# Performance work log

Measured on AMD Instinct MI355X. Metric: run time of the kernel, lower is better.

## Reference

```python
import jax, jax.numpy as jnp
import numpy as np

N, K, M, D = 50000, 32, 50000, 128  # dst nodes, neighbors, src nodes, hidden_dim


def setup_inputs() -> dict:
    key = jax.random.key(0)
    k1, k2, k3, k4 = jax.random.split(key, 4)
    nei = jax.random.randint(k1, (N, K), 0, M, dtype=jnp.int64)
    h = jax.random.normal(k2, (M, D), dtype=jnp.float32)
    h_refer = jax.random.normal(k3, (N, D), dtype=jnp.float32)
    # xavier_normal_ on (1, 2D) with gain=1.414: std = gain*sqrt(2/(1+2D))
    std = 1.414 * np.sqrt(2.0 / (1 + 2 * D))
    att = jax.random.normal(k4, (1, 2 * D), dtype=jnp.float32) * std
    return {"nei": nei, "h": h, "h_refer": h_refer, "att": att}


def reference(nei, h, h_refer, att):
    # gather neighbor embeddings: [N, K, D]
    nei_emb = h[nei]
    # split att so we never materialize the concatenated [N, K, 2D] tensor:
    # cat([h_refer, nei_emb], -1) @ att.T == h_refer @ att_ref + nei_emb @ att_nei
    att_ref = att[0, :D]   # [D]
    att_nei = att[0, D:]   # [D]
    scores = (h_refer @ att_ref)[:, None] + jnp.einsum("nkd,d->nk", nei_emb, att_nei)  # [N, K]
    scores = jax.nn.leaky_relu(scores, negative_slope=0.01)
    w = jax.nn.softmax(scores, axis=1)  # softmax over neighbors
    # weighted sum over neighbors -> [N, D]
    return jnp.einsum("nk,nkd->nd", w, nei_emb)
```

## Files before the change

kernel.cpp:

```cpp
#include <hip/hip_runtime.h>

typedef unsigned int uint32;
typedef unsigned long long uint64;
typedef unsigned short ushort_t;
typedef _Float16 h2_t __attribute__((ext_vector_type(2)));
typedef float  f32x2 __attribute__((ext_vector_type(2)));
typedef float  f32x4 __attribute__((ext_vector_type(4)));
typedef uint32 u32x2 __attribute__((ext_vector_type(2)));

#define KNEI 32
#define DIM 128
#define WPB 4
#define RPW 2
#define WAVE_LDS 8192

enum { SRC_BF16 = 0, SRC_F16 = 1, SRC_F32 = 2 };

__device__ __forceinline__ float bflo(uint32 u) {
    union { uint32 u; float f; } c; c.u = u << 16; return c.f;
}
__device__ __forceinline__ float bfhi(uint32 u) {
    union { uint32 u; float f; } c; c.u = u & 0xffff0000u; return c.f;
}
__device__ __forceinline__ uint32 pack_bf16_rne(float a, float b) {
    union { float f; uint32 u; } x, y; x.f = a; y.f = b;
    uint32 ua = (x.u + 0x7fffu + ((x.u >> 16) & 1u)) >> 16;
    uint32 ub = (y.u + 0x7fffu + ((y.u >> 16) & 1u)) >> 16;
    return (ua & 0xffffu) | (ub << 16);
}
__device__ __forceinline__ uint32 pack_f16(float a, float b) {
    union { h2_t h; uint32 u; } c;
    c.h.x = (_Float16)a; c.h.y = (_Float16)b;
    return c.u;
}
__device__ __forceinline__ h2_t as_h2(uint32 u) {
    union { uint32 u; h2_t h; } c; c.u = u; return c.h;
}

__device__ __forceinline__ void prefetch16(const void* g, void* l) {
    __builtin_amdgcn_global_load_lds(
        (const __attribute__((address_space(1))) void*)g,
        (__attribute__((address_space(3))) void*)l,
        16, 0, 0);
}

__device__ __forceinline__ bool probe_bf16(const void* h, int lane) {
    const uint32 hs = ((const uint32*)h)[lane];
    const uint32 e  = (hs >> 7) & 0xFFu;
    const bool  tb  = (e >= 90u) && (e <= 140u);
    return (__ballot(tb) == ~0ull);
}

template<int SRC>
__device__ __forceinline__ float dot8(const uint4 e, const float* an) {
    if constexpr (SRC == SRC_BF16) {
        return bflo(e.x) * an[0] + bfhi(e.x) * an[1]
             + bflo(e.y) * an[2] + bfhi(e.y) * an[3]
             + bflo(e.z) * an[4] + bfhi(e.z) * an[5]
             + bflo(e.w) * an[6] + bfhi(e.w) * an[7];
    } else {
        const h2_t e0 = as_h2(e.x), e1 = as_h2(e.y), e2 = as_h2(e.z), e3 = as_h2(e.w);
        const float t0 = fmaf((float)e0.x, an[0],
                         fmaf((float)e0.y, an[1],
                         fmaf((float)e1.x, an[2], (float)e1.y * an[3])));
        const float t1 = fmaf((float)e2.x, an[4],
                         fmaf((float)e2.y, an[5],
                         fmaf((float)e3.x, an[6], (float)e3.y * an[7])));
        return t0 + t1;
    }
}

template<int SRC>
__device__ __forceinline__ void acc8(float* acc, float wk, const uint4 e) {
    if constexpr (SRC == SRC_BF16) {
        acc[0] = fmaf(wk, bflo(e.x), acc[0]);
        acc[1] = fmaf(wk, bfhi(e.x), acc[1]);
        acc[2] = fmaf(wk, bflo(e.y), acc[2]);
        acc[3] = fmaf(wk, bfhi(e.y), acc[3]);
        acc[4] = fmaf(wk, bflo(e.z), acc[4]);
        acc[5] = fmaf(wk, bfhi(e.z), acc[5]);
        acc[6] = fmaf(wk, bflo(e.w), acc[6]);
        acc[7] = fmaf(wk, bfhi(e.w), acc[7]);
    } else {
        const h2_t e0 = as_h2(e.x), e1 = as_h2(e.y), e2 = as_h2(e.z), e3 = as_h2(e.w);
        acc[0] = fmaf(wk, (float)e0.x, acc[0]);
        acc[1] = fmaf(wk, (float)e0.y, acc[1]);
        acc[2] = fmaf(wk, (float)e1.x, acc[2]);
        acc[3] = fmaf(wk, (float)e1.y, acc[3]);
        acc[4] = fmaf(wk, (float)e2.x, acc[4]);
        acc[5] = fmaf(wk, (float)e2.y, acc[5]);
        acc[6] = fmaf(wk, (float)e3.x, acc[6]);
        acc[7] = fmaf(wk, (float)e3.y, acc[7]);
    }
}

template<int SRC>
__device__ __forceinline__ f32x2 process_row(
    const uint4* ev, const float* an, float base, int r4)
{
    float s[8];
    #pragma unroll
    for (int it = 0; it < 8; ++it) s[it] = dot8<SRC>(ev[it], an);
    #pragma unroll
    for (int off = 1; off <= 8; off <<= 1) {
        #pragma unroll
        for (int it = 0; it < 8; ++it)
            s[it] += __shfl_xor(s[it], off, 64);
    }
    #pragma unroll
    for (int it = 0; it < 8; ++it) {
        const float v = base + s[it];
        s[it] = (v > 0.f) ? v : 0.01f * v;
    }

    float m = fmaxf(fmaxf(fmaxf(s[0], s[1]), fmaxf(s[2], s[3])),
                    fmaxf(fmaxf(s[4], s[5]), fmaxf(s[6], s[7])));
    m = fmaxf(m, __shfl_xor(m, 16, 64));
    m = fmaxf(m, __shfl_xor(m, 32, 64));

    float w[8];
    #pragma unroll
    for (int it = 0; it < 8; ++it) w[it] = __expf(s[it] - m);
    float sum = ((w[0] + w[1]) + (w[2] + w[3])) + ((w[4] + w[5]) + (w[6] + w[7]));
    sum += __shfl_xor(sum, 16, 64);
    sum += __shfl_xor(sum, 32, 64);
    const float inv = 1.0f / sum;

    float acc[8] = {0.f, 0.f, 0.f, 0.f, 0.f, 0.f, 0.f, 0.f};
    #pragma unroll
    for (int it = 0; it < 8; ++it)
        acc8<SRC>(acc, w[it] * inv, ev[it]);

    const bool b1 = (r4 & 2) != 0;
    const bool b0 = (r4 & 1) != 0;
    float t[4];
    #pragma unroll
    for (int j = 0; j < 4; ++j) {
        const float keep = b1 ? acc[4 + j] : acc[j];
        const float send = b1 ? acc[j]     : acc[4 + j];
        t[j] = keep + __shfl_xor(send, 32, 64);
    }
    f32x2 o;
    {
        const float k0 = b0 ? t[2] : t[0];
        const float s0 = b0 ? t[0] : t[2];
        o.x = k0 + __shfl_xor(s0, 16, 64);
        const float k1 = b0 ? t[3] : t[1];
        const float s1 = b0 ? t[1] : t[3];
        o.y = k1 + __shfl_xor(s1, 16, 64);
    }
    return o;
}

template<int SRC>
__device__ __forceinline__ void run_two(
    const void* __restrict__ hsv, const void* __restrict__ hrv,
    const void* __restrict__ attv, void* __restrict__ outv,
    const void* __restrict__ neiv, bool i64, int Mrows,
    size_t n0, bool valid2, int lane, char* wbase)
{
    constexpr bool F32 = (SRC != SRC_BF16);
    const int r4 = lane >> 4;
    const int c  = lane & 15;

    const size_t ebase = n0 * KNEI;
    const int esel = valid2 ? lane : (lane & 31);
    int idxv;
    if (i64) idxv = (int)__builtin_nontemporal_load((const long long*)neiv + ebase + esel);
    else     idxv = __builtin_nontemporal_load((const int*)neiv + ebase + esel);
    idxv = min(max(idxv, 0), Mrows - 1);

    const int r2 = lane >> 5, l5 = lane & 31;
    const size_t brow = n0 + (valid2 ? (size_t)r2 : 0);
    float hb[4], ab[4];
    if (F32) {
        const f32x4 hp = __builtin_nontemporal_load(
            (const f32x4*)((const float*)hrv + brow * DIM) + l5);
        const f32x4 ap = *((const f32x4*)attv + l5);
        hb[0] = hp.x; hb[1] = hp.y; hb[2] = hp.z; hb[3] = hp.w;
        ab[0] = ap.x; ab[1] = ap.y; ab[2] = ap.z; ab[3] = ap.w;
    } else {
        const u32x2 hu = __builtin_nontemporal_load(
            (const u32x2*)((const ushort_t*)hrv + brow * DIM) + l5);
        const u32x2 au = *((const u32x2*)attv + l5);
        hb[0] = bflo(hu.x); hb[1] = bfhi(hu.x); hb[2] = bflo(hu.y); hb[3] = bfhi(hu.y);
        ab[0] = bflo(au.x); ab[1] = bfhi(au.x); ab[2] = bflo(au.y); ab[3] = bfhi(au.y);
    }

    float an[8];
    if (F32) {
        const float4* ap = (const float4*)((const float*)attv + DIM + c * 8);
        const float4 p0 = ap[0], p1 = ap[1];
        an[0] = p0.x; an[1] = p0.y; an[2] = p0.z; an[3] = p0.w;
        an[4] = p1.x; an[5] = p1.y; an[6] = p1.z; an[7] = p1.w;
    } else {
        const uint4 au = *((const uint4*)((const ushort_t*)attv + DIM) + c);
        an[0] = bflo(au.x); an[1] = bfhi(au.x); an[2] = bflo(au.y); an[3] = bfhi(au.y);
        an[4] = bflo(au.z); an[5] = bfhi(au.z); an[6] = bflo(au.w); an[7] = bfhi(au.w);
    }

    int rows_a[8], rows_b[8];
    #pragma unroll
    for (int it = 0; it < 8; ++it) {
        rows_a[it] = __shfl(idxv, it * 4 + r4, 64);
        rows_b[it] = __shfl(idxv, 32 + it * 4 + r4, 64);
    }

    uint4 evA[8];
    #pragma unroll
    for (int it = 0; it < 8; ++it) {
        if constexpr (SRC == SRC_F32) {
            const float4* sp = (const float4*)hsv + ((size_t)rows_a[it] << 5) + c * 2;
            const float4 p0 = sp[0], p1 = sp[1];
            evA[it].x = pack_f16(p0.x, p0.y);
            evA[it].y = pack_f16(p0.z, p0.w);
            evA[it].z = pack_f16(p1.x, p1.y);
            evA[it].w = pack_f16(p1.z, p1.w);
        } else {
            evA[it] = *((const uint4*)hsv + ((size_t)rows_a[it] << 4) + c);
        }
    }

    if constexpr (SRC != SRC_F32) {
        #pragma unroll
        for (int it = 0; it < 8; ++it)
            prefetch16((const uint4*)hsv + ((size_t)rows_b[it] << 4) + c,
                       wbase + it * 1024);
    }

    float bsum = hb[0] * ab[0] + hb[1] * ab[1] + hb[2] * ab[2] + hb[3] * ab[3];
    #pragma unroll
    for (int off = 1; off <= 16; off <<= 1)
        bsum += __shfl_xor(bsum, off, 64);
    const float baseA = __shfl(bsum, 0, 64);
    const float baseB = __shfl(bsum, 32, 64);

    const f32x2 oA = process_row<SRC>(evA, an, baseA, r4);

    f32x2 oB;
    if constexpr (SRC == SRC_F32) {
        uint4 evB[8];
        #pragma unroll
        for (int it = 0; it < 8; ++it) {
            const float4* sp = (const float4*)hsv + ((size_t)rows_b[it] << 5) + c * 2;
            const float4 p0 = sp[0], p1 = sp[1];
            evB[it].x = pack_f16(p0.x, p0.y);
            evB[it].y = pack_f16(p0.z, p0.w);
            evB[it].z = pack_f16(p1.x, p1.y);
            evB[it].w = pack_f16(p1.z, p1.w);
        }
        oB = process_row<SRC>(evB, an, baseB, r4);
    } else {
        __builtin_amdgcn_sched_barrier(0);
        asm volatile("s_waitcnt vmcnt(0)" ::: "memory");
        uint4 evB[8];
        #pragma unroll
        for (int it = 0; it < 8; ++it)
            evB[it] = *(const uint4*)(wbase + it * 1024 + lane * 16);
        oB = process_row<SRC>(evB, an, baseB, r4);
    }

    if (F32) {
        __builtin_nontemporal_store(oA, (f32x2*)((float*)outv + n0 * DIM) + c * 4 + r4);
        if (valid2)
            __builtin_nontemporal_store(oB, (f32x2*)((float*)outv + (n0 + 1) * DIM) + c * 4 + r4);
    } else {
        __builtin_nontemporal_store(pack_bf16_rne(oA.x, oA.y),
            (uint32*)((ushort_t*)outv + n0 * DIM) + c * 4 + r4);
        if (valid2)
            __builtin_nontemporal_store(pack_bf16_rne(oB.x, oB.y),
                (uint32*)((ushort_t*)outv + (n0 + 1) * DIM) + c * 4 + r4);
    }
}

__global__ __launch_bounds__(256, 8) void gat_kernel(
    const void* __restrict__ nei, const void* __restrict__ h,
    const void* __restrict__ h_refer, const void* __restrict__ att,
    void* __restrict__ out, const void* __restrict__ hf16,
    int N, int Mrows, int use_ws)
{
    __shared__ __align__(16) char smem[WPB * WAVE_LDS];
    const int tid  = threadIdx.x;
    const int lane = tid & 63;
    const int wave = tid >> 6;
    const size_t n0 = ((size_t)blockIdx.x * WPB + wave) * RPW;

    const bool is_bf16 = probe_bf16(h, lane);
    const uint32 nhi = ((const uint32*)nei)[2 * lane + 1];
    const bool  i64  = (__ballot(nhi == 0u) == ~0ull);

    if (n0 >= (size_t)N) return;
    const bool valid2 = (n0 + 1 < (size_t)N);
    char* wbase = smem + wave * WAVE_LDS;

    if (is_bf16)     run_two<SRC_BF16>(h,    h_refer, att, out, nei, i64, Mrows, n0, valid2, lane, wbase);
    else if (use_ws) run_two<SRC_F16 >(hf16, h_refer, att, out, nei, i64, Mrows, n0, valid2, lane, wbase);
    else             run_two<SRC_F32 >(h,    h_refer, att, out, nei, i64, Mrows, n0, valid2, lane, wbase);
}

__global__ __launch_bounds__(256) void conv_kernel(
    const void* __restrict__ h, uint4* __restrict__ ws, long long ngroups)
{
    if (probe_bf16(h, threadIdx.x & 63)) return;
    const long long i = (long long)blockIdx.x * 256 + threadIdx.x;
    if (i >= ngroups) return;
    const f32x4* sp = (const f32x4*)h + i * 2;
    const f32x4 p0 = __builtin_nontemporal_load(sp);
    const f32x4 p1 = __builtin_nontemporal_load(sp + 1);
    uint4 o;
    o.x = pack_f16(p0.x, p0.y);
    o.y = pack_f16(p0.z, p0.w);
    o.z = pack_f16(p1.x, p1.y);
    o.w = pack_f16(p1.z, p1.w);
    ws[i] = o;
}

extern "C" void kernel_launch(void* const* d_in, const int* in_sizes, int n_in,
                              void* d_out, int out_size, void* d_ws, size_t ws_size,
                              hipStream_t stream) {
    const int N = out_size / DIM;
    const int M = in_sizes[1] / DIM;

    const size_t need = (size_t)M * DIM * sizeof(ushort_t);
    const int use_ws = (d_ws != nullptr && ws_size >= need) ? 1 : 0;

    if (use_ws) {
        const long long ngroups = (long long)M * (DIM / 8);
        dim3 cg((unsigned)((ngroups + 255) / 256)), cb(256);
        conv_kernel<<<cg, cb, 0, stream>>>(d_in[1], (uint4*)d_ws, ngroups);
    }

    const int rows_per_block = WPB * RPW;
    dim3 grid((N + rows_per_block - 1) / rows_per_block), block(64 * WPB);
    gat_kernel<<<grid, block, 0, stream>>>(d_in[0], d_in[1], d_in[2], d_in[3],
                                           d_out, d_ws, N, M, use_ws);
}
```

Baseline: 166.3 us.

## Double-buffer neighbor gathers through LDS over four rows per wave

Each wave now handles four destination rows instead of two, staging every row's neighbor tile into one of two LDS buffers with global_load_lds. The next tile's gather is issued while the current one is computed, with partial vmcnt waits between them. The aim is to hide gather latency behind the score and softmax work. In exchange, blocks shrink to two waves with twice the LDS per wave, which may lower occupancy, and the fallback path for f32 without a workspace is rewritten as a simple per-row loop.

```diff
diff --git a/kernel.cpp b/kernel.cpp
--- a/kernel.cpp
+++ b/kernel.cpp
@@ -6,13 +6,14 @@
 typedef _Float16 h2_t __attribute__((ext_vector_type(2)));
 typedef float  f32x2 __attribute__((ext_vector_type(2)));
 typedef float  f32x4 __attribute__((ext_vector_type(4)));
-typedef uint32 u32x2 __attribute__((ext_vector_type(2)));
+typedef uint32 u32x4 __attribute__((ext_vector_type(4)));
 
 #define KNEI 32
 #define DIM 128
-#define WPB 4
-#define RPW 2
-#define WAVE_LDS 8192
+#define WPB 2
+#define CH  4
+#define TILE_BYTES 8192
+#define WAVE_LDS (2 * TILE_BYTES)
 
 enum { SRC_BF16 = 0, SRC_F16 = 1, SRC_F32 = 2 };
 
@@ -42,6 +43,15 @@
         (const __attribute__((address_space(1))) void*)g,
         (__attribute__((address_space(3))) void*)l,
         16, 0, 0);
+}
+
+__device__ __forceinline__ void wait_vm8() {
+    asm volatile("s_waitcnt vmcnt(8)" ::: "memory");
+    __builtin_amdgcn_sched_barrier(0);
+}
+__device__ __forceinline__ void wait_vm0() {
+    asm volatile("s_waitcnt vmcnt(0)" ::: "memory");
+    __builtin_amdgcn_sched_barrier(0);
 }
 
 __device__ __forceinline__ bool probe_bf16(const void* h, int lane) {
@@ -152,40 +162,71 @@
     return o;
 }
 
+template<int HALF>
+__device__ __forceinline__ void stage_tile(const void* __restrict__ hsv,
+                                           int idxreg, int r4, int c, char* buf) {
+    #pragma unroll
+    for (int it = 0; it < 8; ++it) {
+        const int row = __shfl(idxreg, HALF * 32 + it * 4 + r4, 64);
+        prefetch16((const uint4*)hsv + ((size_t)row << 4) + c, buf + it * 1024);
+    }
+}
+
 template<int SRC>
-__device__ __forceinline__ void run_two(
+__device__ __forceinline__ void run_chunk_lds(
     const void* __restrict__ hsv, const void* __restrict__ hrv,
     const void* __restrict__ attv, void* __restrict__ outv,
     const void* __restrict__ neiv, bool i64, int Mrows,
-    size_t n0, bool valid2, int lane, char* wbase)
+    size_t n0, int N, int lane, char* wbase)
 {
     constexpr bool F32 = (SRC != SRC_BF16);
     const int r4 = lane >> 4;
     const int c  = lane & 15;
-
-    const size_t ebase = n0 * KNEI;
-    const int esel = valid2 ? lane : (lane & 31);
-    int idxv;
-    if (i64) idxv = (int)__builtin_nontemporal_load((const long long*)neiv + ebase + esel);
-    else     idxv = __builtin_nontemporal_load((const int*)neiv + ebase + esel);
-    idxv = min(max(idxv, 0), Mrows - 1);
-
-    const int r2 = lane >> 5, l5 = lane & 31;
-    const size_t brow = n0 + (valid2 ? (size_t)r2 : 0);
-    float hb[4], ab[4];
+    const size_t nlast = (size_t)(N - 1);
+
+    const size_t rA = (n0 + (size_t)(lane >> 5)     <= nlast) ? n0 + (lane >> 5)     : nlast;
+    const size_t rB = (n0 + 2 + (size_t)(lane >> 5) <= nlast) ? n0 + 2 + (lane >> 5) : nlast;
+    int idx01, idx23;
+    if (i64) {
+        idx01 = (int)__builtin_nontemporal_load((const long long*)neiv + rA * KNEI + (lane & 31));
+        idx23 = (int)__builtin_nontemporal_load((const long long*)neiv + rB * KNEI + (lane & 31));
+    } else {
+        idx01 = __builtin_nontemporal_load((const int*)neiv + rA * KNEI + (lane & 31));
+        idx23 = __builtin_nontemporal_load((const int*)neiv + rB * KNEI + (lane & 31));
+    }
+    idx01 = min(max(idx01, 0), Mrows - 1);
+    idx23 = min(max(idx23, 0), Mrows - 1);
+
+    stage_tile<0>(hsv, idx01, r4, c, wbase);
+    stage_tile<1>(hsv, idx01, r4, c, wbase + TILE_BYTES);
+
+    const int g = lane >> 4, j = lane & 15;
+    const size_t brow = (n0 + (size_t)g <= nlast) ? n0 + g : nlast;
+    float bsum;
     if (F32) {
-        const f32x4 hp = __builtin_nontemporal_load(
-            (const f32x4*)((const float*)hrv + brow * DIM) + l5);
-        const f32x4 ap = *((const f32x4*)attv + l5);
-        hb[0] = hp.x; hb[1] = hp.y; hb[2] = hp.z; hb[3] = hp.w;
-        ab[0] = ap.x; ab[1] = ap.y; ab[2] = ap.z; ab[3] = ap.w;
+        const f32x4* hp = (const f32x4*)((const float*)hrv + brow * DIM + j * 8);
+        const f32x4* ap = (const f32x4*)((const float*)attv + j * 8);
+        const f32x4 h0 = __builtin_nontemporal_load(hp);
+        const f32x4 h1 = __builtin_nontemporal_load(hp + 1);
+        const f32x4 a0 = ap[0], a1 = ap[1];
+        bsum = h0.x * a0.x + h0.y * a0.y + h0.z * a0.z + h0.w * a0.w
+             + h1.x * a1.x + h1.y * a1.y + h1.z * a1.z + h1.w * a1.w;
     } else {
-        const u32x2 hu = __builtin_nontemporal_load(
-            (const u32x2*)((const ushort_t*)hrv + brow * DIM) + l5);
-        const u32x2 au = *((const u32x2*)attv + l5);
-        hb[0] = bflo(hu.x); hb[1] = bfhi(hu.x); hb[2] = bflo(hu.y); hb[3] = bfhi(hu.y);
-        ab[0] = bflo(au.x); ab[1] = bfhi(au.x); ab[2] = bflo(au.y); ab[3] = bfhi(au.y);
-    }
+        const u32x4 hu = __builtin_nontemporal_load(
+            (const u32x4*)((const ushort_t*)hrv + brow * DIM + j * 8));
+        const u32x4 au = *(const u32x4*)((const ushort_t*)attv + j * 8);
+        bsum = bflo(hu.x) * bflo(au.x) + bfhi(hu.x) * bfhi(au.x)
+             + bflo(hu.y) * bflo(au.y) + bfhi(hu.y) * bfhi(au.y)
+             + bflo(hu.z) * bflo(au.z) + bfhi(hu.z) * bfhi(au.z)
+             + bflo(hu.w) * bflo(au.w) + bfhi(hu.w) * bfhi(au.w);
+    }
+    #pragma unroll
+    for (int off = 1; off <= 8; off <<= 1)
+        bsum += __shfl_xor(bsum, off, 64);
+    float base[CH];
+    #pragma unroll
+    for (int i = 0; i < CH; ++i)
+        base[i] = __shfl(bsum, i << 4, 64);
 
     float an[8];
     if (F32) {
@@ -199,81 +240,106 @@
         an[4] = bflo(au.z); an[5] = bfhi(au.z); an[6] = bflo(au.w); an[7] = bfhi(au.w);
     }
 
-    int rows_a[8], rows_b[8];
-    #pragma unroll
-    for (int it = 0; it < 8; ++it) {
-        rows_a[it] = __shfl(idxv, it * 4 + r4, 64);
-        rows_b[it] = __shfl(idxv, 32 + it * 4 + r4, 64);
-    }
-
-    uint4 evA[8];
-    #pragma unroll
-    for (int it = 0; it < 8; ++it) {
-        if constexpr (SRC == SRC_F32) {
-            const float4* sp = (const float4*)hsv + ((size_t)rows_a[it] << 5) + c * 2;
-            const float4 p0 = sp[0], p1 = sp[1];
-            evA[it].x = pack_f16(p0.x, p0.y);
-            evA[it].y = pack_f16(p0.z, p0.w);
-            evA[it].z = pack_f16(p1.x, p1.y);
-            evA[it].w = pack_f16(p1.z, p1.w);
-        } else {
-            evA[it] = *((const uint4*)hsv + ((size_t)rows_a[it] << 4) + c);
+    f32x2 o[CH];
+    uint4 ev[8];
+    const int lb = lane * 16;
+
+    wait_vm8();
+    #pragma unroll
+    for (int it = 0; it < 8; ++it) ev[it] = *(const uint4*)(wbase + it * 1024 + lb);
+    o[0] = process_row<SRC>(ev, an, base[0], r4);
+    __builtin_amdgcn_sched_barrier(0);
+    stage_tile<0>(hsv, idx23, r4, c, wbase);
+
+    wait_vm8();
+    #pragma unroll
+    for (int it = 0; it < 8; ++it) ev[it] = *(const uint4*)(wbase + TILE_BYTES + it * 1024 + lb);
+    o[1] = process_row<SRC>(ev, an, base[1], r4);
+    __builtin_amdgcn_sched_barrier(0);
+    stage_tile<1>(hsv, idx23, r4, c, wbase + TILE_BYTES);
+
+    wait_vm8();
+    #pragma unroll
+    for (int it = 0; it < 8; ++it) ev[it] = *(const uint4*)(wbase + it * 1024 + lb);
+    o[2] = process_row<SRC>(ev, an, base[2], r4);
+
+    wait_vm0();
+    #pragma unroll
+    for (int it = 0; it < 8; ++it) ev[it] = *(const uint4*)(wbase + TILE_BYTES + it * 1024 + lb);
+    o[3] = process_row<SRC>(ev, an, base[3], r4);
+
+    const int soff = c * 4 + r4;
+    #pragma unroll
+    for (int i = 0; i < CH; ++i) {
+        if (n0 + (size_t)i <= nlast) {
+            if (F32) {
+                __builtin_nontemporal_store(o[i],
+                    (f32x2*)((float*)outv + (n0 + i) * DIM) + soff);
+            } else {
+                __builtin_nontemporal_store(pack_bf16_rne(o[i].x, o[i].y),
+                    (uint32*)((ushort_t*)outv + (n0 + i) * DIM) + soff);
+            }
         }
     }
-
-    if constexpr (SRC != SRC_F32) {
-        #pragma unroll
-        for (int it = 0; it < 8; ++it)
-            prefetch16((const uint4*)hsv + ((size_t)rows_b[it] << 4) + c,
-                       wbase + it * 1024);
-    }
-
-    float bsum = hb[0] * ab[0] + hb[1] * ab[1] + hb[2] * ab[2] + hb[3] * ab[3];
-    #pragma unroll
-    for (int off = 1; off <= 16; off <<= 1)
-        bsum += __shfl_xor(bsum, off, 64);
-    const float baseA = __shfl(bsum, 0, 64);
-    const float baseB = __shfl(bsum, 32, 64);
-
-    const f32x2 oA = process_row<SRC>(evA, an, baseA, r4);
-
-    f32x2 oB;
-    if constexpr (SRC == SRC_F32) {
-        uint4 evB[8];
+}
+
+__device__ __forceinline__ void run_chunk_f32(
+    const void* __restrict__ hsv, const void* __restrict__ hrv,
+    const void* __restrict__ attv, void* __restrict__ outv,
+    const void* __restrict__ neiv, bool i64, int Mrows,
+    size_t n0, int N, int lane)
+{
+    const int r4 = lane >> 4;
+    const int c  = lane & 15;
+    const size_t nlast = (size_t)(N - 1);
+
+    float an[8];
+    {
+        const float4* ap = (const float4*)((const float*)attv + DIM + c * 8);
+        const float4 p0 = ap[0], p1 = ap[1];
+        an[0] = p0.x; an[1] = p0.y; an[2] = p0.z; an[3] = p0.w;
+        an[4] = p1.x; an[5] = p1.y; an[6] = p1.z; an[7] = p1.w;
+    }
+
+    for (int i = 0; i < CH; ++i) {
+        const size_t n = (n0 + (size_t)i <= nlast) ? n0 + i : nlast;
+        int idxv;
+        if (i64) idxv = (int)((const long long*)neiv)[n * KNEI + (lane & 31)];
+        else     idxv = ((const int*)neiv)[n * KNEI + (lane & 31)];
+        idxv = min(max(idxv, 0), Mrows - 1);
+
+        uint4 ev[8];
         #pragma unroll
         for (int it = 0; it < 8; ++it) {
-            const float4* sp = (const float4*)hsv + ((size_t)rows_b[it] << 5) + c * 2;
+            const int row = __shfl(idxv, it * 4 + r4, 64);
+            const float4* sp = (const float4*)hsv + ((size_t)row << 5) + c * 2;
             const float4 p0 = sp[0], p1 = sp[1];
-            evB[it].x = pack_f16(p0.x, p0.y);
-            evB[it].y = pack_f16(p0.z, p0.w);
-            evB[it].z = pack_f16(p1.x, p1.y);
-            evB[it].w = pack_f16(p1.z, p1.w);
+            ev[it].x = pack_f16(p0.x, p0.y);
+            ev[it].y = pack_f16(p0.z, p0.w);
+            ev[it].z = pack_f16(p1.x, p1.y);
+            ev[it].w = pack_f16(p1.z, p1.w);
         }
-        oB = process_row<SRC>(evB, an, baseB, r4);
-    } else {
-        __builtin_amdgcn_sched_barrier(0);
-        asm volatile("s_waitcnt vmcnt(0)" ::: "memory");
-        uint4 evB[8];
+
+        float bsum;
+        {
+            const f32x4 hp = *((const f32x4*)((const float*)hrv + n * DIM) + (lane & 31));
+            const f32x4 ap2 = *((const f32x4*)attv + (lane & 31));
+            bsum = hp.x * ap2.x + hp.y * ap2.y + hp.z * ap2.z + hp.w * ap2.w;
+        }
         #pragma unroll
-        for (int it = 0; it < 8; ++it)
-            evB[it] = *(const uint4*)(wbase + it * 1024 + lane * 16);
-        oB = process_row<SRC>(evB, an, baseB, r4);
-    }
-
-    if (F32) {
-        __builtin_nontemporal_store(oA, (f32x2*)((float*)outv + n0 * DIM) + c * 4 + r4);
-        if (valid2)
-            __builtin_nontemporal_store(oB, (f32x2*)((float*)outv + (n0 + 1) * DIM) + c * 4 + r4);
-    } else {
-        __builtin_nontemporal_store(pack_bf16_rne(oA.x, oA.y),
-            (uint32*)((ushort_t*)outv + n0 * DIM) + c * 4 + r4);
-        if (valid2)
-            __builtin_nontemporal_store(pack_bf16_rne(oB.x, oB.y),
-                (uint32*)((ushort_t*)outv + (n0 + 1) * DIM) + c * 4 + r4);
-    }
-}
-
-__global__ __launch_bounds__(256, 8) void gat_kernel(
+        for (int off = 1; off <= 16; off <<= 1)
+            bsum += __shfl_xor(bsum, off, 64);
+        const float base = __shfl(bsum, 0, 64);
+
+        const f32x2 o = process_row<SRC_F32>(ev, an, base, r4);
+        if (n0 + (size_t)i <= nlast) {
+            f32x2 ov; ov.x = o.x; ov.y = o.y;
+            *((f32x2*)((float*)outv + n * DIM) + c * 4 + r4) = ov;
+        }
+    }
+}
+
+__global__ __launch_bounds__(64 * WPB) void gat_kernel(
     const void* __restrict__ nei, const void* __restrict__ h,
     const void* __restrict__ h_refer, const void* __restrict__ att,
     void* __restrict__ out, const void* __restrict__ hf16,
@@ -283,19 +349,18 @@
     const int tid  = threadIdx.x;
     const int lane = tid & 63;
     const int wave = tid >> 6;
-    const size_t n0 = ((size_t)blockIdx.x * WPB + wave) * RPW;
+    const size_t n0 = ((size_t)blockIdx.x * WPB + wave) * CH;
 
     const bool is_bf16 = probe_bf16(h, lane);
     const uint32 nhi = ((const uint32*)nei)[2 * lane + 1];
     const bool  i64  = (__ballot(nhi == 0u) == ~0ull);
 
     if (n0 >= (size_t)N) return;
-    const bool valid2 = (n0 + 1 < (size_t)N);
     char* wbase = smem + wave * WAVE_LDS;
 
-    if (is_bf16)     run_two<SRC_BF16>(h,    h_refer, att, out, nei, i64, Mrows, n0, valid2, lane, wbase);
-    else if (use_ws) run_two<SRC_F16 >(hf16, h_refer, att, out, nei, i64, Mrows, n0, valid2, lane, wbase);
-    else             run_two<SRC_F32 >(h,    h_refer, att, out, nei, i64, Mrows, n0, valid2, lane, wbase);
+    if (is_bf16)     run_chunk_lds<SRC_BF16>(h,    h_refer, att, out, nei, i64, Mrows, n0, N, lane, wbase);
+    else if (use_ws) run_chunk_lds<SRC_F16 >(hf16, h_refer, att, out, nei, i64, Mrows, n0, N, lane, wbase);
+    else             run_chunk_f32(h, h_refer, att, out, nei, i64, Mrows, n0, N, lane);
 }
 
 __global__ __launch_bounds__(256) void conv_kernel(
@@ -330,7 +395,7 @@
         conv_kernel<<<cg, cb, 0, stream>>>(d_in[1], (uint4*)d_ws, ngroups);
     }
 
-    const int rows_per_block = WPB * RPW;
+    const int rows_per_block = WPB * CH;
     dim3 grid((N + rows_per_block - 1) / rows_per_block), block(64 * WPB);
     gat_kernel<<<grid, block, 0, stream>>>(d_in[0], d_in[1], d_in[2], d_in[3],
                                            d_out, d_ws, N, M, use_ws);
```

Measured after the change: 202.2 us. +21.6%, slower.
